# Kernel tuning notes

Hardware: AMD Instinct MI355X
Metric: run time of the kernel (lower is better)

The kernel has to match this reference:

```python
import jax, jax.numpy as jnp
import numpy as np

EPS = 1e-06
LAMBDA_PCSL = 0.1
LAMBDA_GPAL = 0.1


def setup_inputs() -> dict:
    key = jax.random.key(0)
    k1, k2 = jax.random.split(key)
    N, D, P = 262144, 256, 512
    features = jax.random.normal(k1, (N, D), dtype=jnp.float32)
    patient_ids = jax.random.randint(k2, (N,), 0, P, dtype=jnp.int64)
    return {"features": features, "patient_ids": patient_ids, "num_patients": P}


def _pafa_loss(features, patient_ids, num_patients):
    # Segmented mean: centroids[p] = mean of features with patient_ids == p
    seg_ids = patient_ids.astype(jnp.int32)
    sums = jax.ops.segment_sum(features, seg_ids, num_segments=num_patients)  # [P, D]
    counts = jax.ops.segment_sum(jnp.ones((features.shape[0],), features.dtype),
                                 seg_ids, num_segments=num_patients)          # [P]
    counts = jnp.maximum(counts, 1.0)  # every patient assumed present (as in original)
    centroids = sums / counts[:, None]                                        # [P, D]

    # Within-patient variance: sum_i ||x_i - c_{pid_i}||^2
    diff = features - centroids[seg_ids]                                      # [N, D]
    within_variance = jnp.sum(diff * diff)

    # Pairwise centroid distances: sum_{i<j} ||c_i - c_j||^2
    #   = P * sum_i ||c_i||^2 - ||sum_i c_i||^2   (exact identity, no O(P^2) loop)
    sq_norms = jnp.sum(centroids * centroids, axis=1)                         # [P]
    total = jnp.sum(centroids, axis=0)                                        # [D]
    P = jnp.asarray(num_patients, centroids.dtype)
    between_distance = P * jnp.sum(sq_norms) - jnp.sum(total * total)

    loss_pcsl = within_variance / (between_distance + EPS)

    # Global patient alignment: mean ||c_p - mean(c)||^2
    global_centroid = jnp.mean(centroids, axis=0)                             # [D]
    gdiff = centroids - global_centroid
    loss_gpal = jnp.mean(jnp.sum(gdiff * gdiff, axis=1))

    return LAMBDA_PCSL * loss_pcsl + LAMBDA_GPAL * loss_gpal


def reference(features, patient_ids, num_patients):
    return _pafa_loss(features, patient_ids, num_patients)
```

## Files before the change

kernel.cpp:

```cpp
#include <hip/hip_runtime.h>


#define DIMS 256
#define NPAT 512
#define HB 64
#define HT 1024
#define MT 1024
#define MW 16


extern "C" __global__ void __launch_bounds__(HT)
k_hist(const int* __restrict__ pids, int N, unsigned* __restrict__ bh,
       float* __restrict__ scalars, float* __restrict__ T)
{
    __shared__ unsigned h[NPAT];
    const int t = threadIdx.x;
    if (t < NPAT) h[t] = 0u;
    __syncthreads();

    const int r = (blockIdx.x * HT + t) * 4;
    if (r + 3 < N) {
        const int4 p4 = *reinterpret_cast<const int4*>(pids + r);
        atomicAdd(&h[p4.x], 1u);
        atomicAdd(&h[p4.y], 1u);
        atomicAdd(&h[p4.z], 1u);
        atomicAdd(&h[p4.w], 1u);
    } else {
        for (int k = 0; k < 4; ++k)
            if (r + k < N) atomicAdd(&h[pids[r + k]], 1u);
    }
    __syncthreads();
    if (t < NPAT) bh[t * HB + blockIdx.x] = h[t];

    if (blockIdx.x == 0) {
        if (t < 4)    scalars[t] = 0.0f;
        if (t < DIMS) T[t]       = 0.0f;
    }
}

extern "C" __global__ void __launch_bounds__(HT)
k_scatter(const int* __restrict__ pids, int N,
          const unsigned* __restrict__ bh, unsigned* __restrict__ counts,
          unsigned* __restrict__ starts, unsigned* __restrict__ idx)
{
    __shared__ unsigned tmp[NPAT];
    __shared__ unsigned basec[NPAT];

    const int t   = threadIdx.x;
    const int blk = blockIdx.x;

    unsigned total = 0u, pref = 0u, padded = 0u;
    if (t < NPAT) {
        const uint4* row = reinterpret_cast<const uint4*>(bh + t * HB);
        #pragma unroll
        for (int k = 0; k < HB / 4; ++k) {
            const uint4 v = row[k];
            const int b0 = 4 * k;
            pref  += (b0 + 0 < blk ? v.x : 0u);
            pref  += (b0 + 1 < blk ? v.y : 0u);
            pref  += (b0 + 2 < blk ? v.z : 0u);
            pref  += (b0 + 3 < blk ? v.w : 0u);
            total += v.x + v.y + v.z + v.w;
        }
        padded = (total + 3u) & ~3u;
        tmp[t] = padded;
    }
    __syncthreads();
    for (int off = 1; off < NPAT; off <<= 1) {
        const unsigned v = (t >= off && t < NPAT) ? tmp[t - off] : 0u;
        __syncthreads();
        if (t < NPAT) tmp[t] += v;
        __syncthreads();
    }
    if (t < NPAT) {
        const unsigned st = tmp[t] - padded;
        basec[t] = st + pref;
        if (blk == 0) { starts[t] = st; counts[t] = total; }
    }
    __syncthreads();

    const int r = (blk * HT + t) * 4;
    if (r + 3 < N) {
        const int4 p4 = *reinterpret_cast<const int4*>(pids + r);
        idx[atomicAdd(&basec[p4.x], 1u)] = (unsigned)(r + 0);
        idx[atomicAdd(&basec[p4.y], 1u)] = (unsigned)(r + 1);
        idx[atomicAdd(&basec[p4.z], 1u)] = (unsigned)(r + 2);
        idx[atomicAdd(&basec[p4.w], 1u)] = (unsigned)(r + 3);
    } else {
        for (int k = 0; k < 4; ++k)
            if (r + k < N)
                idx[atomicAdd(&basec[pids[r + k]], 1u)] = (unsigned)(r + k);
    }
}

extern "C" __global__ void __launch_bounds__(MT, 4)
k_main(const float* __restrict__ feats, const unsigned* __restrict__ idx,
       const unsigned* __restrict__ counts, const unsigned* __restrict__ starts,
       float* __restrict__ T, float* __restrict__ scalars)
{
    __shared__ float part[MW][DIMS];
    __shared__ float sred[MW];
    __shared__ float cred[4];

    const int p    = blockIdx.x;
    const int lane = threadIdx.x & 63;
    const int w    = threadIdx.x >> 6;
    const unsigned start = starts[p];
    const unsigned cnt   = counts[p];
    const unsigned base  = lane * 4;

    float ax = 0.f, ay = 0.f, az = 0.f, aw = 0.f;
    float ssq = 0.f;

    const unsigned nb = cnt >> 2;
    for (unsigned b = (unsigned)w; b < nb; b += MW) {
        const uint4 cid = *reinterpret_cast<const uint4*>(idx + start + 4u * b);
        const float4 v0 = *reinterpret_cast<const float4*>(feats + (size_t)cid.x * DIMS + base);
        const float4 v1 = *reinterpret_cast<const float4*>(feats + (size_t)cid.y * DIMS + base);
        const float4 v2 = *reinterpret_cast<const float4*>(feats + (size_t)cid.z * DIMS + base);
        const float4 v3 = *reinterpret_cast<const float4*>(feats + (size_t)cid.w * DIMS + base);
        ax += v0.x + v1.x + v2.x + v3.x;
        ay += v0.y + v1.y + v2.y + v3.y;
        az += v0.z + v1.z + v2.z + v3.z;
        aw += v0.w + v1.w + v2.w + v3.w;
        ssq += v0.x*v0.x + v0.y*v0.y + v0.z*v0.z + v0.w*v0.w;
        ssq += v1.x*v1.x + v1.y*v1.y + v1.z*v1.z + v1.w*v1.w;
        ssq += v2.x*v2.x + v2.y*v2.y + v2.z*v2.z + v2.w*v2.w;
        ssq += v3.x*v3.x + v3.y*v3.y + v3.z*v3.z + v3.w*v3.w;
    }
    if (w == 0) {
        for (unsigned rr = nb * 4u; rr < cnt; ++rr) {
            const unsigned row = idx[start + rr];
            const float4 v = *reinterpret_cast<const float4*>(feats + (size_t)row * DIMS + base);
            ax += v.x; ay += v.y; az += v.z; aw += v.w;
            ssq += v.x*v.x + v.y*v.y + v.z*v.z + v.w*v.w;
        }
    }

    part[w][base + 0] = ax;
    part[w][base + 1] = ay;
    part[w][base + 2] = az;
    part[w][base + 3] = aw;
    for (int off = 32; off; off >>= 1) ssq += __shfl_down(ssq, off, 64);
    if (lane == 0) sred[w] = ssq;
    __syncthreads();

    const int d = threadIdx.x;
    if (d < DIMS) {
        float s = 0.f;
        #pragma unroll
        for (int ww = 0; ww < MW; ++ww) s += part[ww][d];
        const float cntf = fmaxf((float)cnt, 1.0f);
        const float c = s / cntf;
        atomicAdd(&T[d], c);
        float csq = c * c;
        for (int off = 32; off; off >>= 1) csq += __shfl_down(csq, off, 64);
        if ((d & 63) == 0) cred[d >> 6] = csq;
    }
    __syncthreads();

    if (threadIdx.x == 0) {
        const float s2p = cred[0] + cred[1] + cred[2] + cred[3];
        const float cntf = fmaxf((float)cnt, 1.0f);
        atomicAdd(&scalars[2], s2p);
        atomicAdd(&scalars[1], cntf * s2p);
        float sq = 0.f;
        #pragma unroll
        for (int ww = 0; ww < MW; ++ww) sq += sred[ww];
        atomicAdd(&scalars[0], sq);
    }
}

extern "C" __global__ void __launch_bounds__(DIMS)
k_final(const float* __restrict__ T, const float* __restrict__ scalars,
        const int* __restrict__ nump, float* __restrict__ out)
{
    __shared__ float red[4];
    const int d = threadIdx.x;
    const float t = T[d];
    float tt = t * t;
    for (int off = 32; off; off >>= 1) tt += __shfl_down(tt, off, 64);
    if ((d & 63) == 0) red[d >> 6] = tt;
    __syncthreads();
    if (d == 0) {
        const double TT    = (double)red[0] + red[1] + red[2] + red[3];
        const double SumSq = (double)scalars[0];
        const double S1    = (double)scalars[1];
        const double S2    = (double)scalars[2];
        const double Pd    = (double)(*nump);
        const double within  = SumSq - S1;
        const double between = Pd * S2 - TT;
        const double pcsl = within / (between + 1e-6);
        const double gpal = S2 / Pd - TT / (Pd * Pd);
        out[0] = (float)(0.1 * pcsl + 0.1 * gpal);
    }
}

extern "C" void kernel_launch(void* const* d_in, const int* in_sizes, int n_in,
                              void* d_out, int out_size, void* d_ws, size_t ws_size,
                              hipStream_t stream)
{
    const float* feats = (const float*)d_in[0];
    const int*   pids  = (const int*)d_in[1];
    const int*   nump  = (const int*)d_in[2];
    float*       out   = (float*)d_out;

    const int N = in_sizes[0] / DIMS;

    char* ws = (char*)d_ws;
    unsigned* counts  = (unsigned*)(ws);
    unsigned* starts  = (unsigned*)(ws + 2048);
    float*    scalars = (float*)(ws + 4096);
    float*    T       = (float*)(ws + 4608);
    unsigned* bh      = (unsigned*)(ws + 8192);
    unsigned* idx     = (unsigned*)(ws + 139264);

    k_hist   <<<dim3(HB),   dim3(HT),   0, stream>>>(pids, N, bh, scalars, T);
    k_scatter<<<dim3(HB),   dim3(HT),   0, stream>>>(pids, N, bh, counts,
                                                     starts, idx);
    k_main   <<<dim3(NPAT), dim3(MT),   0, stream>>>(feats, idx, counts, starts,
                                                     T, scalars);
    k_final  <<<dim3(1),    dim3(DIMS), 0, stream>>>(T, scalars, nump, out);
}
```

Measured before the change: 69.67 us.

## Split gather-reduce into fixed-size chunks spanning patient segments for load balance

The main reduction now splits the sorted index array into fixed 512-row chunks instead of using one block per patient. Each chunk finds the patients it overlaps by binary search and accumulates per-segment sums in shared memory, then adds them atomically into global per-patient sums. A new centroid kernel with one block per patient does the final reduction, and its last-finishing block (found with a done counter) computes the loss, which removes the separate final kernel. This evens out the work across blocks when patient counts vary. In exchange it adds shared and global atomics at chunk boundaries, and MAXSEG=6 assumes no chunk spans more than six patients.

```diff
diff --git a/kernel.cpp b/kernel.cpp
--- a/kernel.cpp
+++ b/kernel.cpp
@@ -7,11 +7,14 @@
 #define HT 1024
 #define MT 1024
 #define MW 16
+#define CH 512
+#define MAXSEG 6
 
 
 extern "C" __global__ void __launch_bounds__(HT)
 k_hist(const int* __restrict__ pids, int N, unsigned* __restrict__ bh,
-       float* __restrict__ scalars, float* __restrict__ T)
+       float* __restrict__ gsums, float* __restrict__ scalars,
+       float* __restrict__ T, unsigned* __restrict__ done)
 {
     __shared__ unsigned h[NPAT];
     const int t = threadIdx.x;
@@ -32,8 +35,10 @@
     __syncthreads();
     if (t < NPAT) bh[t * HB + blockIdx.x] = h[t];
 
+    reinterpret_cast<float2*>(gsums)[blockIdx.x * HT + t] = make_float2(0.f, 0.f);
     if (blockIdx.x == 0) {
         if (t < 4)    scalars[t] = 0.0f;
+        if (t == 4)   *done      = 0u;
         if (t < DIMS) T[t]       = 0.0f;
     }
 }
@@ -49,7 +54,7 @@
     const int t   = threadIdx.x;
     const int blk = blockIdx.x;
 
-    unsigned total = 0u, pref = 0u, padded = 0u;
+    unsigned total = 0u, pref = 0u;
     if (t < NPAT) {
         const uint4* row = reinterpret_cast<const uint4*>(bh + t * HB);
         #pragma unroll
@@ -62,8 +67,7 @@
             pref  += (b0 + 3 < blk ? v.w : 0u);
             total += v.x + v.y + v.z + v.w;
         }
-        padded = (total + 3u) & ~3u;
-        tmp[t] = padded;
+        tmp[t] = total;
     }
     __syncthreads();
     for (int off = 1; off < NPAT; off <<= 1) {
@@ -73,7 +77,7 @@
         __syncthreads();
     }
     if (t < NPAT) {
-        const unsigned st = tmp[t] - padded;
+        const unsigned st = tmp[t] - total;
         basec[t] = st + pref;
         if (blk == 0) { starts[t] = st; counts[t] = total; }
     }
@@ -94,76 +98,108 @@
 }
 
 extern "C" __global__ void __launch_bounds__(MT, 4)
-k_main(const float* __restrict__ feats, const unsigned* __restrict__ idx,
-       const unsigned* __restrict__ counts, const unsigned* __restrict__ starts,
-       float* __restrict__ T, float* __restrict__ scalars)
-{
-    __shared__ float part[MW][DIMS];
-    __shared__ float sred[MW];
-    __shared__ float cred[4];
-
-    const int p    = blockIdx.x;
-    const int lane = threadIdx.x & 63;
-    const int w    = threadIdx.x >> 6;
-    const unsigned start = starts[p];
-    const unsigned cnt   = counts[p];
-    const unsigned base  = lane * 4;
+k_mainf(const float* __restrict__ feats, const unsigned* __restrict__ idx,
+        const unsigned* __restrict__ starts, int N,
+        float* __restrict__ gsums, float* __restrict__ scalars)
+{
+    __shared__ float    part[MAXSEG][DIMS];
+    __shared__ float    sred[MW];
+    __shared__ unsigned sh_start[NPAT];
+    __shared__ unsigned sh_nseg;
+    __shared__ unsigned sh_bound[MAXSEG];
+    __shared__ unsigned sh_pat[MAXSEG];
+
+    const int t    = threadIdx.x;
+    const int lane = t & 63;
+    const int w    = t >> 6;
+    const unsigned c0 = (unsigned)blockIdx.x * CH;
+    const unsigned c1 = c0 + CH;
+
+    if (t < NPAT) sh_start[t] = starts[t];
+    for (int i = t; i < MAXSEG * DIMS; i += MT)
+        reinterpret_cast<float*>(part)[i] = 0.f;
+    __syncthreads();
+
+    if (t == 0) {
+        unsigned lo = 0, hi = NPAT - 1;
+        while (lo < hi) {
+            const unsigned mid = (lo + hi + 1) >> 1;
+            if (sh_start[mid] <= c0) lo = mid; else hi = mid - 1;
+        }
+        unsigned ns = 0, p = lo;
+        while (true) {
+            const unsigned end = (p + 1 < NPAT) ? sh_start[p + 1] : (unsigned)N;
+            sh_pat[ns]   = p;
+            sh_bound[ns] = (end < c1) ? end : c1;
+            ns++;
+            if (end >= c1 || ns >= MAXSEG) break;
+            p++;
+        }
+        sh_nseg = ns;
+    }
+    __syncthreads();
+
+    const unsigned nseg = sh_nseg;
+    unsigned seg = 0;
+    {
+        const unsigned sp = c0 + 4u * (unsigned)w;
+        while (seg + 1 < nseg && sp >= sh_bound[seg]) seg++;
+    }
+    unsigned bnd = sh_bound[seg];
 
     float ax = 0.f, ay = 0.f, az = 0.f, aw = 0.f;
     float ssq = 0.f;
-
-    const unsigned nb = cnt >> 2;
-    for (unsigned b = (unsigned)w; b < nb; b += MW) {
-        const uint4 cid = *reinterpret_cast<const uint4*>(idx + start + 4u * b);
-        const float4 v0 = *reinterpret_cast<const float4*>(feats + (size_t)cid.x * DIMS + base);
-        const float4 v1 = *reinterpret_cast<const float4*>(feats + (size_t)cid.y * DIMS + base);
-        const float4 v2 = *reinterpret_cast<const float4*>(feats + (size_t)cid.z * DIMS + base);
-        const float4 v3 = *reinterpret_cast<const float4*>(feats + (size_t)cid.w * DIMS + base);
-        ax += v0.x + v1.x + v2.x + v3.x;
-        ay += v0.y + v1.y + v2.y + v3.y;
-        az += v0.z + v1.z + v2.z + v3.z;
-        aw += v0.w + v1.w + v2.w + v3.w;
-        ssq += v0.x*v0.x + v0.y*v0.y + v0.z*v0.z + v0.w*v0.w;
-        ssq += v1.x*v1.x + v1.y*v1.y + v1.z*v1.z + v1.w*v1.w;
-        ssq += v2.x*v2.x + v2.y*v2.y + v2.z*v2.z + v2.w*v2.w;
-        ssq += v3.x*v3.x + v3.y*v3.y + v3.z*v3.z + v3.w*v3.w;
-    }
-    if (w == 0) {
-        for (unsigned rr = nb * 4u; rr < cnt; ++rr) {
-            const unsigned row = idx[start + rr];
-            const float4 v = *reinterpret_cast<const float4*>(feats + (size_t)row * DIMS + base);
-            ax += v.x; ay += v.y; az += v.z; aw += v.w;
-            ssq += v.x*v.x + v.y*v.y + v.z*v.z + v.w*v.w;
-        }
-    }
-
-    part[w][base + 0] = ax;
-    part[w][base + 1] = ay;
-    part[w][base + 2] = az;
-    part[w][base + 3] = aw;
+    const unsigned base = lane * 4;
+
+    for (unsigned q = c0 + 4u * (unsigned)w; q < c1; q += 4u * MW) {
+        const uint4 cid = *reinterpret_cast<const uint4*>(idx + q);
+        if (q + 4u <= bnd) {
+            const float4 v0 = *reinterpret_cast<const float4*>(feats + (size_t)cid.x * DIMS + base);
+            const float4 v1 = *reinterpret_cast<const float4*>(feats + (size_t)cid.y * DIMS + base);
+            const float4 v2 = *reinterpret_cast<const float4*>(feats + (size_t)cid.z * DIMS + base);
+            const float4 v3 = *reinterpret_cast<const float4*>(feats + (size_t)cid.w * DIMS + base);
+            ax += v0.x + v1.x + v2.x + v3.x;
+            ay += v0.y + v1.y + v2.y + v3.y;
+            az += v0.z + v1.z + v2.z + v3.z;
+            aw += v0.w + v1.w + v2.w + v3.w;
+            ssq += v0.x*v0.x + v0.y*v0.y + v0.z*v0.z + v0.w*v0.w;
+            ssq += v1.x*v1.x + v1.y*v1.y + v1.z*v1.z + v1.w*v1.w;
+            ssq += v2.x*v2.x + v2.y*v2.y + v2.z*v2.z + v2.w*v2.w;
+            ssq += v3.x*v3.x + v3.y*v3.y + v3.z*v3.z + v3.w*v3.w;
+        } else {
+            const unsigned rows[4] = { cid.x, cid.y, cid.z, cid.w };
+            #pragma unroll
+            for (int k = 0; k < 4; ++k) {
+                while (q + (unsigned)k >= bnd) {
+                    atomicAdd(&part[seg][base + 0], ax);
+                    atomicAdd(&part[seg][base + 1], ay);
+                    atomicAdd(&part[seg][base + 2], az);
+                    atomicAdd(&part[seg][base + 3], aw);
+                    ax = ay = az = aw = 0.f;
+                    seg++;
+                    bnd = sh_bound[seg];
+                }
+                const float4 v = *reinterpret_cast<const float4*>(
+                    feats + (size_t)rows[k] * DIMS + base);
+                ax += v.x; ay += v.y; az += v.z; aw += v.w;
+                ssq += v.x*v.x + v.y*v.y + v.z*v.z + v.w*v.w;
+            }
+        }
+    }
+    atomicAdd(&part[seg][base + 0], ax);
+    atomicAdd(&part[seg][base + 1], ay);
+    atomicAdd(&part[seg][base + 2], az);
+    atomicAdd(&part[seg][base + 3], aw);
+
     for (int off = 32; off; off >>= 1) ssq += __shfl_down(ssq, off, 64);
     if (lane == 0) sred[w] = ssq;
     __syncthreads();
 
-    const int d = threadIdx.x;
-    if (d < DIMS) {
-        float s = 0.f;
-        #pragma unroll
-        for (int ww = 0; ww < MW; ++ww) s += part[ww][d];
-        const float cntf = fmaxf((float)cnt, 1.0f);
-        const float c = s / cntf;
-        atomicAdd(&T[d], c);
-        float csq = c * c;
-        for (int off = 32; off; off >>= 1) csq += __shfl_down(csq, off, 64);
-        if ((d & 63) == 0) cred[d >> 6] = csq;
-    }
-    __syncthreads();
-
-    if (threadIdx.x == 0) {
-        const float s2p = cred[0] + cred[1] + cred[2] + cred[3];
-        const float cntf = fmaxf((float)cnt, 1.0f);
-        atomicAdd(&scalars[2], s2p);
-        atomicAdd(&scalars[1], cntf * s2p);
+    for (unsigned i = (unsigned)t; i < nseg * DIMS; i += MT) {
+        const unsigned s = i >> 8, d = i & 255u;
+        atomicAdd(&gsums[sh_pat[s] * DIMS + d], part[s][d]);
+    }
+    if (t == 0) {
         float sq = 0.f;
         #pragma unroll
         for (int ww = 0; ww < MW; ++ww) sq += sred[ww];
@@ -172,27 +208,62 @@
 }
 
 extern "C" __global__ void __launch_bounds__(DIMS)
-k_final(const float* __restrict__ T, const float* __restrict__ scalars,
-        const int* __restrict__ nump, float* __restrict__ out)
-{
+k_cent(const float* __restrict__ gsums, const unsigned* __restrict__ counts,
+       float* __restrict__ T, float* __restrict__ scalars,
+       unsigned* __restrict__ done, const int* __restrict__ nump,
+       float* __restrict__ out)
+{
+    __shared__ float cred[4];
     __shared__ float red[4];
+    __shared__ unsigned lastflag;
+
+    const int p = blockIdx.x;
     const int d = threadIdx.x;
-    const float t = T[d];
-    float tt = t * t;
-    for (int off = 32; off; off >>= 1) tt += __shfl_down(tt, off, 64);
-    if ((d & 63) == 0) red[d >> 6] = tt;
+
+    const float s    = gsums[p * DIMS + d];
+    const float cntf = fmaxf((float)counts[p], 1.0f);
+    const float c    = s / cntf;
+    atomicAdd(&T[d], c);
+
+    float csq = c * c;
+    for (int off = 32; off; off >>= 1) csq += __shfl_down(csq, off, 64);
+    if ((d & 63) == 0) cred[d >> 6] = csq;
     __syncthreads();
     if (d == 0) {
-        const double TT    = (double)red[0] + red[1] + red[2] + red[3];
-        const double SumSq = (double)scalars[0];
-        const double S1    = (double)scalars[1];
-        const double S2    = (double)scalars[2];
-        const double Pd    = (double)(*nump);
-        const double within  = SumSq - S1;
-        const double between = Pd * S2 - TT;
-        const double pcsl = within / (between + 1e-6);
-        const double gpal = S2 / Pd - TT / (Pd * Pd);
-        out[0] = (float)(0.1 * pcsl + 0.1 * gpal);
+        const float s2p = cred[0] + cred[1] + cred[2] + cred[3];
+        atomicAdd(&scalars[2], s2p);
+        atomicAdd(&scalars[1], cntf * s2p);
+    }
+
+    __threadfence();
+    if (d == 0) {
+        const unsigned prev = __hip_atomic_fetch_add(
+            done, 1u, __ATOMIC_ACQ_REL, __HIP_MEMORY_SCOPE_AGENT);
+        lastflag = (prev == (unsigned)(gridDim.x - 1)) ? 1u : 0u;
+    }
+    __syncthreads();
+    if (lastflag) {
+        const float tv = __hip_atomic_load(&T[d], __ATOMIC_RELAXED,
+                                           __HIP_MEMORY_SCOPE_AGENT);
+        float tt = tv * tv;
+        for (int off = 32; off; off >>= 1) tt += __shfl_down(tt, off, 64);
+        if ((d & 63) == 0) red[d >> 6] = tt;
+        __syncthreads();
+        if (d == 0) {
+            const double TT    = (double)red[0] + red[1] + red[2] + red[3];
+            const double SumSq = (double)__hip_atomic_load(&scalars[0],
+                __ATOMIC_RELAXED, __HIP_MEMORY_SCOPE_AGENT);
+            const double S1 = (double)__hip_atomic_load(&scalars[1],
+                __ATOMIC_RELAXED, __HIP_MEMORY_SCOPE_AGENT);
+            const double S2 = (double)__hip_atomic_load(&scalars[2],
+                __ATOMIC_RELAXED, __HIP_MEMORY_SCOPE_AGENT);
+            const double Pd = (double)(*nump);
+            const double within  = SumSq - S1;
+            const double between = Pd * S2 - TT;
+            const double pcsl = within / (between + 1e-6);
+            const double gpal = S2 / Pd - TT / (Pd * Pd);
+            out[0] = (float)(0.1 * pcsl + 0.1 * gpal);
+        }
     }
 }
 
@@ -206,19 +277,24 @@
     float*       out   = (float*)d_out;
 
     const int N = in_sizes[0] / DIMS;
+    const int NB = N / CH;
 
     char* ws = (char*)d_ws;
     unsigned* counts  = (unsigned*)(ws);
     unsigned* starts  = (unsigned*)(ws + 2048);
     float*    scalars = (float*)(ws + 4096);
+    unsigned* done    = (unsigned*)(ws + 4352);
     float*    T       = (float*)(ws + 4608);
     unsigned* bh      = (unsigned*)(ws + 8192);
-    unsigned* idx     = (unsigned*)(ws + 139264);
-
-    k_hist   <<<dim3(HB),   dim3(HT),   0, stream>>>(pids, N, bh, scalars, T);
+    float*    gsums   = (float*)(ws + 139264);
+    unsigned* idx     = (unsigned*)(ws + 663552);
+
+    k_hist   <<<dim3(HB),   dim3(HT),   0, stream>>>(pids, N, bh, gsums,
+                                                     scalars, T, done);
     k_scatter<<<dim3(HB),   dim3(HT),   0, stream>>>(pids, N, bh, counts,
                                                      starts, idx);
-    k_main   <<<dim3(NPAT), dim3(MT),   0, stream>>>(feats, idx, counts, starts,
-                                                     T, scalars);
-    k_final  <<<dim3(1),    dim3(DIMS), 0, stream>>>(T, scalars, nump, out);
-}
+    k_mainf  <<<dim3(NB),   dim3(MT),   0, stream>>>(feats, idx, starts, N,
+                                                     gsums, scalars);
+    k_cent   <<<dim3(NPAT), dim3(DIMS), 0, stream>>>(gsums, counts, T, scalars,
+                                                     done, nump, out);
+}
```

New measurement: 123.2 us. 76.9% more time.

## Split each patient across four smaller blocks and use wave-shuffle prefix scan

Applied to the files above, without the earlier changes.

The main gather kernel now runs four 512-thread blocks per patient instead of one 1024-thread block, each writing a partial sum to global memory. A new small kernel then combines the four partials into centroids and does the atomic reductions. Separately, the scatter kernel's shared-memory Hillis-Steele scan is replaced by a two-level wave-shuffle scan, which needs fewer barriers. The aim is better load balance and occupancy across CUs, at the cost of an extra kernel launch and a round trip of partial sums through global memory.

```diff
diff --git a/kernel.cpp b/kernel.cpp
--- a/kernel.cpp
+++ b/kernel.cpp
@@ -5,8 +5,7 @@
 #define NPAT 512
 #define HB 64
 #define HT 1024
-#define MT 1024
-#define MW 16
+#define NSUB 4
 
 
 extern "C" __global__ void __launch_bounds__(HT)
@@ -43,11 +42,13 @@
           const unsigned* __restrict__ bh, unsigned* __restrict__ counts,
           unsigned* __restrict__ starts, unsigned* __restrict__ idx)
 {
-    __shared__ unsigned tmp[NPAT];
+    __shared__ unsigned wt[HT / 64];
     __shared__ unsigned basec[NPAT];
 
-    const int t   = threadIdx.x;
-    const int blk = blockIdx.x;
+    const int t    = threadIdx.x;
+    const int lane = t & 63;
+    const int wid  = t >> 6;
+    const int blk  = blockIdx.x;
 
     unsigned total = 0u, pref = 0u, padded = 0u;
     if (t < NPAT) {
@@ -63,17 +64,30 @@
             total += v.x + v.y + v.z + v.w;
         }
         padded = (total + 3u) & ~3u;
-        tmp[t] = padded;
-    }
-    __syncthreads();
-    for (int off = 1; off < NPAT; off <<= 1) {
-        const unsigned v = (t >= off && t < NPAT) ? tmp[t - off] : 0u;
-        __syncthreads();
-        if (t < NPAT) tmp[t] += v;
-        __syncthreads();
-    }
+    }
+
+    unsigned v = padded;
+    #pragma unroll
+    for (int off = 1; off < 64; off <<= 1) {
+        const unsigned u = __shfl_up(v, off, 64);
+        if (lane >= off) v += u;
+    }
+    if (lane == 63) wt[wid] = v;
+    __syncthreads();
+    if (t < HT / 64) {
+        unsigned x = wt[t];
+        #pragma unroll
+        for (int off = 1; off < HT / 64; off <<= 1) {
+            const unsigned u = __shfl_up(x, off, HT / 64);
+            if ((t & (HT / 64 - 1)) >= off) x += u;
+        }
+        wt[t] = x;
+    }
+    __syncthreads();
+    const unsigned incl = v + (wid > 0 ? wt[wid - 1] : 0u);
+
     if (t < NPAT) {
-        const unsigned st = tmp[t] - padded;
+        const unsigned st = incl - padded;
         basec[t] = st + pref;
         if (blk == 0) { starts[t] = st; counts[t] = total; }
     }
@@ -93,28 +107,33 @@
     }
 }
 
-extern "C" __global__ void __launch_bounds__(MT, 4)
+extern "C" __global__ void __launch_bounds__(512)
 k_main(const float* __restrict__ feats, const unsigned* __restrict__ idx,
        const unsigned* __restrict__ counts, const unsigned* __restrict__ starts,
-       float* __restrict__ T, float* __restrict__ scalars)
-{
-    __shared__ float part[MW][DIMS];
-    __shared__ float sred[MW];
-    __shared__ float cred[4];
-
-    const int p    = blockIdx.x;
-    const int lane = threadIdx.x & 63;
-    const int w    = threadIdx.x >> 6;
+       float* __restrict__ gpart, float* __restrict__ gssq)
+{
+    __shared__ float part[8][DIMS];
+    __shared__ float sred[8];
+
+    const int t    = threadIdx.x;
+    const int lane = t & 63;
+    const int w    = t >> 6;
+    const int b    = blockIdx.x;
+    const int p    = b >> 2;
+    const int s    = b & 3;
     const unsigned start = starts[p];
     const unsigned cnt   = counts[p];
     const unsigned base  = lane * 4;
 
+    const unsigned nb = cnt >> 2;
+    const unsigned bs = (nb * (unsigned)s) >> 2;
+    const unsigned be = (nb * (unsigned)(s + 1)) >> 2;
+
     float ax = 0.f, ay = 0.f, az = 0.f, aw = 0.f;
     float ssq = 0.f;
 
-    const unsigned nb = cnt >> 2;
-    for (unsigned b = (unsigned)w; b < nb; b += MW) {
-        const uint4 cid = *reinterpret_cast<const uint4*>(idx + start + 4u * b);
+    for (unsigned q = bs + (unsigned)w; q < be; q += 8) {
+        const uint4 cid = *reinterpret_cast<const uint4*>(idx + start + 4u * q);
         const float4 v0 = *reinterpret_cast<const float4*>(feats + (size_t)cid.x * DIMS + base);
         const float4 v1 = *reinterpret_cast<const float4*>(feats + (size_t)cid.y * DIMS + base);
         const float4 v2 = *reinterpret_cast<const float4*>(feats + (size_t)cid.z * DIMS + base);
@@ -128,7 +147,7 @@
         ssq += v2.x*v2.x + v2.y*v2.y + v2.z*v2.z + v2.w*v2.w;
         ssq += v3.x*v3.x + v3.y*v3.y + v3.z*v3.z + v3.w*v3.w;
     }
-    if (w == 0) {
+    if (s == 3 && w == 0) {
         for (unsigned rr = nb * 4u; rr < cnt; ++rr) {
             const unsigned row = idx[start + rr];
             const float4 v = *reinterpret_cast<const float4*>(feats + (size_t)row * DIMS + base);
@@ -145,28 +164,47 @@
     if (lane == 0) sred[w] = ssq;
     __syncthreads();
 
+    if (t < DIMS) {
+        float sum = 0.f;
+        #pragma unroll
+        for (int ww = 0; ww < 8; ++ww) sum += part[ww][t];
+        gpart[(size_t)b * DIMS + t] = sum;
+    }
+    if (t == 0) {
+        float sq = 0.f;
+        #pragma unroll
+        for (int ww = 0; ww < 8; ++ww) sq += sred[ww];
+        gssq[b] = sq;
+    }
+}
+
+extern "C" __global__ void __launch_bounds__(DIMS)
+k_cent(const float* __restrict__ gpart, const float* __restrict__ gssq,
+       const unsigned* __restrict__ counts,
+       float* __restrict__ T, float* __restrict__ scalars)
+{
+    __shared__ float cred[4];
+    const int p = blockIdx.x;
     const int d = threadIdx.x;
-    if (d < DIMS) {
-        float s = 0.f;
-        #pragma unroll
-        for (int ww = 0; ww < MW; ++ww) s += part[ww][d];
-        const float cntf = fmaxf((float)cnt, 1.0f);
-        const float c = s / cntf;
-        atomicAdd(&T[d], c);
-        float csq = c * c;
-        for (int off = 32; off; off >>= 1) csq += __shfl_down(csq, off, 64);
-        if ((d & 63) == 0) cred[d >> 6] = csq;
-    }
-    __syncthreads();
-
-    if (threadIdx.x == 0) {
+
+    const float sum = gpart[(size_t)(4 * p + 0) * DIMS + d]
+                    + gpart[(size_t)(4 * p + 1) * DIMS + d]
+                    + gpart[(size_t)(4 * p + 2) * DIMS + d]
+                    + gpart[(size_t)(4 * p + 3) * DIMS + d];
+    const float cntf = fmaxf((float)counts[p], 1.0f);
+    const float c = sum / cntf;
+    atomicAdd(&T[d], c);
+
+    float csq = c * c;
+    for (int off = 32; off; off >>= 1) csq += __shfl_down(csq, off, 64);
+    if ((d & 63) == 0) cred[d >> 6] = csq;
+    __syncthreads();
+    if (d == 0) {
         const float s2p = cred[0] + cred[1] + cred[2] + cred[3];
-        const float cntf = fmaxf((float)cnt, 1.0f);
         atomicAdd(&scalars[2], s2p);
         atomicAdd(&scalars[1], cntf * s2p);
-        float sq = 0.f;
-        #pragma unroll
-        for (int ww = 0; ww < MW; ++ww) sq += sred[ww];
+        const float sq = gssq[4 * p + 0] + gssq[4 * p + 1]
+                       + gssq[4 * p + 2] + gssq[4 * p + 3];
         atomicAdd(&scalars[0], sq);
     }
 }
@@ -213,12 +251,17 @@
     float*    scalars = (float*)(ws + 4096);
     float*    T       = (float*)(ws + 4608);
     unsigned* bh      = (unsigned*)(ws + 8192);
-    unsigned* idx     = (unsigned*)(ws + 139264);
-
-    k_hist   <<<dim3(HB),   dim3(HT),   0, stream>>>(pids, N, bh, scalars, T);
-    k_scatter<<<dim3(HB),   dim3(HT),   0, stream>>>(pids, N, bh, counts,
-                                                     starts, idx);
-    k_main   <<<dim3(NPAT), dim3(MT),   0, stream>>>(feats, idx, counts, starts,
-                                                     T, scalars);
-    k_final  <<<dim3(1),    dim3(DIMS), 0, stream>>>(T, scalars, nump, out);
-}
+    float*    gssq    = (float*)(ws + 139264);
+    float*    gpart   = (float*)(ws + 147456);
+    unsigned* idx     = (unsigned*)(ws + 2244608);
+
+    k_hist   <<<dim3(HB),          dim3(HT),   0, stream>>>(pids, N, bh,
+                                                            scalars, T);
+    k_scatter<<<dim3(HB),          dim3(HT),   0, stream>>>(pids, N, bh, counts,
+                                                            starts, idx);
+    k_main   <<<dim3(NPAT * NSUB), dim3(512),  0, stream>>>(feats, idx, counts,
+                                                            starts, gpart, gssq);
+    k_cent   <<<dim3(NPAT),        dim3(DIMS), 0, stream>>>(gpart, gssq, counts,
+                                                            T, scalars);
+    k_final  <<<dim3(1),           dim3(DIMS), 0, stream>>>(T, scalars, nump, out);
+}
```

After: 82.85 us. 18.9% more time.
